# Optimization experiments

Measured on AMD Instinct MI355X. Metric: run time of the kernel, lower is better.

## Reference

```python
import jax, jax.numpy as jnp
import numpy as np

MODES = 32
WIDTH = 64


def crelu(z):
    # split-complex ReLU (torch.relu is undefined on complex; this is the standard fix)
    return jax.nn.relu(z.real) + 1j * jax.nn.relu(z.imag)


def _linear_params(key, fan_in, fan_out):
    k1, k2 = jax.random.split(key)
    s = 1.0 / np.sqrt(fan_in)
    W = jax.random.uniform(k1, (fan_out, fan_in), minval=-s, maxval=s, dtype=jnp.float32)
    b = jax.random.uniform(k2, (fan_out,), minval=-s, maxval=s, dtype=jnp.float32)
    return W, b


def setup_inputs() -> dict:
    key = jax.random.key(0)
    ks = jax.random.split(key, 8)
    B, G = 32768, 512
    H0, H1, H2 = 1024, 512, 64  # hidden_layers; H2 == WIDTH
    FD = 128                    # field_dim
    geometry_input = jax.random.normal(ks[0], (B, G), dtype=jnp.float32)
    W_in, b_in = _linear_params(ks[1], G, H0)
    W_h1, b_h1 = _linear_params(ks[2], H0, H1)
    W_h2, b_h2 = _linear_params(ks[3], H1, H2)
    w0 = jax.random.normal(ks[4], (MODES, WIDTH), dtype=jnp.float32)
    w1 = jax.random.normal(ks[5], (MODES, WIDTH), dtype=jnp.float32)
    lin1_W, lin1_b = _linear_params(ks[6], WIDTH, WIDTH)
    k7a, k7b = jax.random.split(ks[7])
    lin2_W, lin2_b = _linear_params(k7a, WIDTH, WIDTH)
    W_out, b_out = _linear_params(k7b, H2, FD)
    return dict(geometry_input=geometry_input, W_in=W_in, b_in=b_in,
                W_h1=W_h1, b_h1=b_h1, W_h2=W_h2, b_h2=b_h2,
                w0=w0, w1=w1, lin1_W=lin1_W, lin1_b=lin1_b,
                lin2_W=lin2_W, lin2_b=lin2_b, W_out=W_out, b_out=b_out)


def reference(geometry_input, W_in, b_in, W_h1, b_h1, W_h2, b_h2,
              w0, w1, lin1_W, lin1_b, lin2_W, lin2_b, W_out, b_out):
    # MLP encoder: [B, G] -> [B, 64]
    x = jax.nn.relu(geometry_input @ W_in.T + b_in)
    x = jax.nn.relu(x @ W_h1.T + b_h1)
    x = jax.nn.relu(x @ W_h2.T + b_h2)
    # FNO block
    xh = jnp.fft.fftn(x)  # fftn over ALL axes, as in torch code -> complex64 [B, 64]
    phase = jnp.exp(1j * 2.0 * jnp.pi * jnp.arange(MODES) / MODES).astype(jnp.complex64)
    y = xh[:, None, :] * w0  # per-mode lift: [B, MODES, WIDTH]
    y = crelu(y)
    y = y * phase[None, :, None]  # diagonal L mode-multiply
    y = jnp.einsum('bmw,mw->bw', y, w1.astype(y.dtype))  # collapse modes -> [B, WIDTH]
    y = crelu(y @ lin1_W.T + lin1_b)  # real weights on complex acts
    y = y @ lin2_W.T + lin2_b
    y = jnp.fft.ifftn(y)  # [B, 64] complex
    out = y @ W_out.T + b_out  # [B, field_dim] complex
    return out
```

## Files before the change

kernel.cpp:

```cpp
#include <hip/hip_runtime.h>
#include <hip/hip_bf16.h>


#define PI2F 6.28318530717958647692f

typedef __attribute__((ext_vector_type(8))) short short8;
typedef __attribute__((ext_vector_type(4))) float f32x4;

__device__ __forceinline__ unsigned short f2bf(float f) {
  unsigned int u = __float_as_uint(f);
  u += 0x7fff + ((u >> 16) & 1);
  return (unsigned short)(u >> 16);
}
__device__ __forceinline__ unsigned int pack_bf16x2(float a, float b) {
  return (unsigned int)f2bf(a) | ((unsigned int)f2bf(b) << 16);
}

__device__ __forceinline__ void gl2lds16(const void* gptr, const void* lptr) {
  __builtin_amdgcn_global_load_lds(
      (const __attribute__((address_space(1))) unsigned int*)(unsigned long long)gptr,
      (__attribute__((address_space(3))) unsigned int*)(unsigned int)(unsigned long long)lptr,
      16, 0, 0);
}

__global__ __launch_bounds__(256) void f32_to_bf16_k(
    const float* __restrict__ src, unsigned short* __restrict__ dst, int n4)
{
  int i = blockIdx.x * 256 + threadIdx.x;
  if (i < n4) {
    float4 v = ((const float4*)src)[i];
    uint2 p;
    p.x = pack_bf16x2(v.x, v.y);
    p.y = pack_bf16x2(v.z, v.w);
    ((uint2*)dst)[i] = p;
  }
}

template<int BM, int BN, int WM, int WN, typename OUT>
__global__ __launch_bounds__(256) void gemm_async(
    const unsigned short* __restrict__ A, const unsigned short* __restrict__ Bw,
    const float* __restrict__ bias, OUT* __restrict__ C,
    int M, int N, int K)
{
  constexpr int BK = 64;
  __shared__ __align__(16) unsigned short lA[BM * BK];
  __shared__ __align__(16) unsigned short lB[BN * BK];
  const int tid = threadIdx.x;
  const int lane = tid & 63;
  const int wv = tid >> 6;
  const int q = lane >> 4, lr = lane & 15;
  const int x7 = lr & 7;
  constexpr int WN_CNT = BN / WN;
  const int wm = (wv / WN_CNT) * WM;
  const int wn = (wv % WN_CNT) * WN;
  const size_t m0 = (size_t)blockIdx.x * BM;
  const size_t n0 = (size_t)blockIdx.y * BN;
  constexpr int MI = WM / 16, NI = WN / 16;
  f32x4 acc[MI][NI] = {};
  constexpr int A_INSTR = BM * BK / 512;
  constexpr int B_INSTR = BN * BK / 512;
  constexpr int A_PW = A_INSTR / 4, B_PW = B_INSTR / 4;
  (void)M;

  for (int k0 = 0; k0 < K; k0 += BK) {
    __syncthreads();
    #pragma unroll
    for (int s = 0; s < A_PW; ++s) {
      int instr = wv * A_PW + s;
      int pc = instr * 64 + lane;
      int row = pc >> 3, col = pc & 7;
      int lc = col ^ (row & 7);
      gl2lds16(A + (m0 + row) * K + k0 + lc * 8, lA + instr * 512);
    }
    #pragma unroll
    for (int s = 0; s < B_PW; ++s) {
      int instr = wv * B_PW + s;
      int pc = instr * 64 + lane;
      int row = pc >> 3, col = pc & 7;
      int lc = col ^ (row & 7);
      gl2lds16(Bw + (n0 + row) * K + k0 + lc * 8, lB + instr * 512);
    }
    __syncthreads();
    #pragma unroll
    for (int t = 0; t < 2; ++t) {
      short8 af[MI], bfr[NI];
      #pragma unroll
      for (int i = 0; i < MI; ++i) {
        int r = wm + i * 16 + lr;
        af[i] = *(const short8*)(lA + r * 64 + (((t << 2) | q) ^ x7) * 8);
      }
      #pragma unroll
      for (int j = 0; j < NI; ++j) {
        int r = wn + j * 16 + lr;
        bfr[j] = *(const short8*)(lB + r * 64 + (((t << 2) | q) ^ x7) * 8);
      }
      #pragma unroll
      for (int i = 0; i < MI; ++i)
        #pragma unroll
        for (int j = 0; j < NI; ++j)
          acc[i][j] = __builtin_amdgcn_mfma_f32_16x16x32_bf16(af[i], bfr[j], acc[i][j], 0, 0, 0);
    }
  }
  #pragma unroll
  for (int i = 0; i < MI; ++i)
    #pragma unroll
    for (int j = 0; j < NI; ++j) {
      size_t col = n0 + wn + j * 16 + lr;
      float bv = bias[col];
      #pragma unroll
      for (int r = 0; r < 4; ++r) {
        size_t row = m0 + wm + i * 16 + q * 4 + r;
        float v = acc[i][j][r] + bv;
        v = v > 0.f ? v : 0.f;
        if (sizeof(OUT) == 2) ((unsigned short*)C)[row * N + col] = f2bf(v);
        else                  ((float*)C)[row * N + col] = v;
      }
    }
}

__global__ __launch_bounds__(256) void precompute(
    const float* __restrict__ w0, const float* __restrict__ w1,
    const float* __restrict__ l2W, const float* __restrict__ l2b,
    float2* __restrict__ Ap, float2* __restrict__ Am,
    float2* __restrict__ Qt, float2* __restrict__ b2c)
{
  const int t = threadIdx.x;
  const int blk = blockIdx.x;
  if (blk == 0) {
    if (t < 64) {
      float apx = 0, apy = 0, amx = 0, amy = 0;
      for (int m = 0; m < 32; ++m) {
        float s0 = w0[m * 64 + t];
        float cf = w1[m * 64 + t] * s0;
        float sn, cs; sincosf(PI2F * (float)m / 32.f, &sn, &cs);
        if (s0 > 0.f)      { apx += cs * cf; apy += sn * cf; }
        else if (s0 < 0.f) { amx += cs * cf; amy += sn * cf; }
      }
      Ap[t] = make_float2(apx, apy);
      Am[t] = make_float2(amx, amy);
      float bx = 0, by = 0;
      for (int k = 0; k < 64; ++k) {
        float sn, cs; sincosf(PI2F * (float)((t * k) & 63) / 64.f, &sn, &cs);
        float lb = l2b[k] * (1.f / 64.f);
        bx += cs * lb; by += sn * lb;
      }
      b2c[t] = make_float2(bx, by);
    }
  } else {
    int e = (blk - 1) * 256 + t;
    int j = e >> 6, w = e & 63;
    float qx = 0, qy = 0;
    for (int k = 0; k < 64; ++k) {
      float sn, cs; sincosf(PI2F * (float)((j * k) & 63) / 64.f, &sn, &cs);
      float lw = l2W[k * 64 + w] * (1.f / 64.f);
      qx += cs * lw; qy += sn * lw;
    }
    Qt[w * 64 + j] = make_float2(qx, qy);
  }
}

__global__ __launch_bounds__(256) void dft64_rows(
    const float* __restrict__ x3, float2* __restrict__ xh1)
{
  __shared__ __align__(16) float xt[32][64];
  __shared__ float2 tw[64];
  const int t = threadIdx.x;
  const size_t b0 = (size_t)blockIdx.x * 32;
  for (int it = 0; it < 8; ++it) {
    int idx = it * 256 + t;
    int r = idx >> 6, w = idx & 63;
    xt[r][w] = x3[(b0 + r) * 64 + w];
  }
  if (t < 64) {
    float sn, cs; sincosf(-PI2F * (float)t / 64.f, &sn, &cs);
    tw[t] = make_float2(cs, sn);
  }
  __syncthreads();
  const int k = t & 63, rg = t >> 6;
  float2 acc[8] = {};
  #pragma unroll 1
  for (int w4 = 0; w4 < 16; ++w4) {
    int w = 4 * w4;
    int kw = k * w;
    float2 t0 = tw[kw & 63];
    float2 t1 = tw[(kw + k) & 63];
    float2 t2 = tw[(kw + 2 * k) & 63];
    float2 t3 = tw[(kw + 3 * k) & 63];
    #pragma unroll
    for (int r = 0; r < 8; ++r) {
      float4 xv = *(const float4*)(&xt[rg * 8 + r][w]);
      acc[r].x += xv.x * t0.x + xv.y * t1.x + xv.z * t2.x + xv.w * t3.x;
      acc[r].y += xv.x * t0.y + xv.y * t1.y + xv.z * t2.y + xv.w * t3.y;
    }
  }
  #pragma unroll
  for (int r = 0; r < 8; ++r)
    xh1[(b0 + rg * 8 + r) * 64 + k] = acc[r];
}

template<int SIGN>
__global__ __launch_bounds__(256) void fft_stage1(
    const float2* __restrict__ Xin, float2* __restrict__ T)
{
  __shared__ float2 tile[128 * 33];
  __shared__ float2 tw16s[16];
  const int blk = blockIdx.x;
  const int b2 = blk >> 1, wh = (blk & 1) * 32;
  const int t = threadIdx.x;
  for (int it = 0; it < 16; ++it) {
    int idx = it * 256 + t;
    int b1 = idx >> 5, wi = idx & 31;
    tile[b1 * 33 + wi] = Xin[((size_t)(b1 * 256 + b2)) * 64 + wh + wi];
  }
  if (t < 16) {
    float sn, cs; sincosf(SIGN * PI2F * (float)t / 16.f, &sn, &cs);
    tw16s[t] = make_float2(cs, sn);
  }
  __syncthreads();
  const int p = t >> 1, n2a = p >> 4, k1pa = p & 15, w0 = (t & 1) * 16;
  float2 ya[16] = {};
  #pragma unroll 1
  for (int n1 = 0; n1 < 16; ++n1) {
    float2 tv = tw16s[(n1 * k1pa) & 15];
    const float2* row = &tile[(8 * n1 + n2a) * 33 + w0];
    #pragma unroll
    for (int w = 0; w < 16; ++w) {
      float2 d = row[w];
      ya[w].x += d.x * tv.x - d.y * tv.y;
      ya[w].y += d.x * tv.y + d.y * tv.x;
    }
  }
  {
    float sn, cs; sincosf(SIGN * PI2F * (float)(n2a * k1pa) / 128.f, &sn, &cs);
    #pragma unroll
    for (int w = 0; w < 16; ++w) {
      float2 a = ya[w];
      ya[w] = make_float2(a.x * cs - a.y * sn, a.x * sn + a.y * cs);
    }
  }
  __syncthreads();
  {
    float2* yrow = &tile[(n2a * 16 + k1pa) * 33 + w0];
    #pragma unroll
    for (int w = 0; w < 16; ++w) yrow[w] = ya[w];
  }
  __syncthreads();
  const int wB = t & 31, qB = t >> 5;
  float sstep, cstep;
  sincosf(SIGN * PI2F * (float)(16 * b2) / 32768.f, &sstep, &cstep);
  #pragma unroll 1
  for (int h = 0; h < 2; ++h) {
    const int k1p = qB + 8 * h;
    float2 acc[8] = {};
    #pragma unroll 1
    for (int n2 = 0; n2 < 8; ++n2) {
      float2 d = tile[(n2 * 16 + k1p) * 33 + wB];
      #pragma unroll
      for (int k2p = 0; k2p < 8; ++k2p) {
        float2 tv = tw16s[(2 * n2 * k2p) & 15];
        acc[k2p].x += d.x * tv.x - d.y * tv.y;
        acc[k2p].y += d.x * tv.y + d.y * tv.x;
      }
    }
    float sb, cb;
    sincosf(SIGN * PI2F * (float)(b2 * k1p) / 32768.f, &sb, &cb);
    float2 rot = make_float2(cb, sb);
    #pragma unroll
    for (int k2p = 0; k2p < 8; ++k2p) {
      int k1 = k1p + 16 * k2p;
      float2 a = acc[k2p];
      float2 o = make_float2(a.x * rot.x - a.y * rot.y,
                             a.x * rot.y + a.y * rot.x);
      T[((size_t)k1 * 256 + b2) * 64 + wh + wB] = o;
      float nrx = rot.x * cstep - rot.y * sstep;
      rot.y = rot.x * sstep + rot.y * cstep;
      rot.x = nrx;
    }
  }
}

template<int SIGN, bool SCALE>
__global__ __launch_bounds__(256) void fft_stage2(
    const float2* __restrict__ T, float2* __restrict__ X)
{
  __shared__ float2 tile[256 * 17];
  __shared__ float2 tw16s[16];
  const int blk = blockIdx.x;
  const int k1 = blk >> 2, wq = (blk & 3) * 16;
  const int t = threadIdx.x;
  for (int it = 0; it < 16; ++it) {
    int idx = it * 256 + t;
    int r2 = idx >> 4, wi = idx & 15;
    tile[r2 * 17 + wi] = T[((size_t)k1 * 256 + r2) * 64 + wq + wi];
  }
  if (t < 16) {
    float sn, cs; sincosf(SIGN * PI2F * (float)t / 16.f, &sn, &cs);
    tw16s[t] = make_float2(cs, sn);
  }
  __syncthreads();
  const int n2a = t >> 4, k1pa = t & 15;
  float2 ya[16] = {};
  #pragma unroll 1
  for (int n1 = 0; n1 < 16; ++n1) {
    float2 tv = tw16s[(n1 * k1pa) & 15];
    const float2* row = &tile[(16 * n1 + n2a) * 17];
    #pragma unroll
    for (int w = 0; w < 16; ++w) {
      float2 d = row[w];
      ya[w].x += d.x * tv.x - d.y * tv.y;
      ya[w].y += d.x * tv.y + d.y * tv.x;
    }
  }
  {
    float sn, cs; sincosf(SIGN * PI2F * (float)(n2a * k1pa) / 256.f, &sn, &cs);
    #pragma unroll
    for (int w = 0; w < 16; ++w) {
      float2 a = ya[w];
      ya[w] = make_float2(a.x * cs - a.y * sn, a.x * sn + a.y * cs);
    }
  }
  __syncthreads();
  {
    float2* yrow = &tile[(n2a * 16 + k1pa) * 17];
    #pragma unroll
    for (int w = 0; w < 16; ++w) yrow[w] = ya[w];
  }
  __syncthreads();
  const int k1pb = t >> 4, wB = t & 15;
  float2 acc[16] = {};
  #pragma unroll 1
  for (int n2 = 0; n2 < 16; ++n2) {
    float2 d = tile[(n2 * 16 + k1pb) * 17 + wB];
    #pragma unroll
    for (int k2p = 0; k2p < 16; ++k2p) {
      float2 tv = tw16s[(n2 * k2p) & 15];
      acc[k2p].x += d.x * tv.x - d.y * tv.y;
      acc[k2p].y += d.x * tv.y + d.y * tv.x;
    }
  }
  const float sc = SCALE ? (1.f / 32768.f) : 1.f;
  #pragma unroll
  for (int k2p = 0; k2p < 16; ++k2p) {
    int k2 = k1pb + 16 * k2p;
    size_t row = (size_t)(k1 + 128 * k2);
    X[row * 64 + wq + wB] = make_float2(acc[k2p].x * sc, acc[k2p].y * sc);
  }
}

__global__ __launch_bounds__(256) void pw_lin(
    const float2* __restrict__ xh,
    const float2* __restrict__ Ap, const float2* __restrict__ Am,
    const float* __restrict__ l1W, const float* __restrict__ l1b,
    const float2* __restrict__ Qt, const float2* __restrict__ b2c,
    float2* __restrict__ u)
{
  __shared__ __align__(16) float2 tile[32][64];
  __shared__ __align__(16) float2 qt[64 * 64];
  const int t = threadIdx.x;
  const int lane = t & 63;
  const int wv = t >> 6;
  const size_t b0 = (size_t)blockIdx.x * 32;

  #pragma unroll
  for (int s = 0; s < 8; ++s) {
    int instr = wv * 8 + s;
    gl2lds16((const char*)Qt + instr * 1024 + lane * 16,
             (const char*)qt + instr * 1024);
  }

  for (int it = 0; it < 8; ++it) {
    int idx = it * 256 + t;
    int r = idx >> 6, w = idx & 63;
    float2 xv = xh[(b0 + r) * 64 + w];
    float2 Aa = (xv.x >= 0.f) ? Ap[w] : Am[w];
    float2 Ab = (xv.y >= 0.f) ? Ap[w] : Am[w];
    tile[r][w] = make_float2(xv.x * Aa.x - xv.y * Ab.y,
                             xv.x * Aa.y + xv.y * Ab.x);
  }
  __syncthreads();

  const int n = lane, rg = wv;

  {
    float2 acc[8] = {};
    const float* wrow = l1W + n * 64;
    float4 lwn = *(const float4*)wrow;
    #pragma unroll 1
    for (int w2 = 0; w2 < 16; ++w2) {
      float4 lw = lwn;
      lwn = *(const float4*)(wrow + 4 * ((w2 + 1) & 15));
      int w = 4 * w2;
      #pragma unroll
      for (int r = 0; r < 8; ++r) {
        const float4* rowp = (const float4*)(&tile[rg * 8 + r][w]);
        float4 y01 = rowp[0];
        float4 y23 = rowp[1];
        acc[r].x += y01.x * lw.x + y01.z * lw.y + y23.x * lw.z + y23.z * lw.w;
        acc[r].y += y01.y * lw.x + y01.w * lw.y + y23.y * lw.z + y23.w * lw.w;
      }
    }
    float bb = l1b[n];
    #pragma unroll
    for (int r = 0; r < 8; ++r) {
      float zr = acc[r].x + bb; zr = zr > 0.f ? zr : 0.f;
      float zi = acc[r].y;      zi = zi > 0.f ? zi : 0.f;
      tile[rg * 8 + r][n] = make_float2(zr, zi);
    }
  }

  {
    const int j = lane;
    float2 acc[8] = {};
    #pragma unroll 1
    for (int w2 = 0; w2 < 16; ++w2) {
      int w = 4 * w2;
      float2 q0 = qt[(w + 0) * 64 + j];
      float2 q1 = qt[(w + 1) * 64 + j];
      float2 q2 = qt[(w + 2) * 64 + j];
      float2 q3 = qt[(w + 3) * 64 + j];
      #pragma unroll
      for (int r = 0; r < 8; ++r) {
        const float4* rowp = (const float4*)(&tile[rg * 8 + r][w]);
        float4 z01 = rowp[0];
        float4 z23 = rowp[1];
        acc[r].x += z01.x * q0.x - z01.y * q0.y
                  + z01.z * q1.x - z01.w * q1.y
                  + z23.x * q2.x - z23.y * q2.y
                  + z23.z * q3.x - z23.w * q3.y;
        acc[r].y += z01.x * q0.y + z01.y * q0.x
                  + z01.z * q1.y + z01.w * q1.x
                  + z23.x * q2.y + z23.y * q2.x
                  + z23.z * q3.y + z23.w * q3.x;
      }
    }
    float2 bc = b2c[j];
    #pragma unroll
    for (int r = 0; r < 8; ++r)
      u[(b0 + rg * 8 + r) * 64 + j] = make_float2(acc[r].x + bc.x, acc[r].y + bc.y);
  }
}

template<int MODE>
__global__ __launch_bounds__(256) void final_out(
    const float2* __restrict__ v, const float* __restrict__ Wout,
    const float* __restrict__ bout, float* __restrict__ out)
{
  __shared__ __align__(16) float2 vt[32][64];
  const int t = threadIdx.x;
  const size_t b0 = (size_t)blockIdx.x * 32;
  for (int it = 0; it < 8; ++it) {
    int idx = it * 256 + t;
    int r = idx >> 6, w = idx & 63;
    vt[r][w] = v[(b0 + r) * 64 + w];
  }
  __syncthreads();
  const int f = t & 127, rg = t >> 7;
  const float* wrow = Wout + f * 64;
  float2 acc[16] = {};
  float2 wvn = *(const float2*)wrow;
  #pragma unroll 1
  for (int j2 = 0; j2 < 32; ++j2) {
    float2 wc = wvn;
    wvn = *(const float2*)(wrow + 2 * ((j2 + 1) & 31));
    #pragma unroll
    for (int r = 0; r < 16; ++r) {
      float4 vv = *(const float4*)(&vt[rg * 16 + r][2 * j2]);
      acc[r].x += vv.x * wc.x + vv.z * wc.y;
      acc[r].y += vv.y * wc.x + vv.w * wc.y;
    }
  }
  float bb = bout[f];
  #pragma unroll
  for (int r = 0; r < 16; ++r) {
    size_t idx = (b0 + rg * 16 + r) * 128 + f;
    if (MODE == 0) out[idx] = acc[r].x + bb;
    else ((float2*)out)[idx] = make_float2(acc[r].x + bb, acc[r].y);
  }
}

extern "C" void kernel_launch(void* const* d_in, const int* in_sizes, int n_in,
                              void* d_out, int out_size, void* d_ws, size_t ws_size,
                              hipStream_t stream)
{
  (void)in_sizes; (void)n_in; (void)ws_size;
  const float* geom = (const float*)d_in[0];
  const float* Win  = (const float*)d_in[1];
  const float* bin  = (const float*)d_in[2];
  const float* Wh1  = (const float*)d_in[3];
  const float* bh1  = (const float*)d_in[4];
  const float* Wh2  = (const float*)d_in[5];
  const float* bh2  = (const float*)d_in[6];
  const float* w0   = (const float*)d_in[7];
  const float* w1   = (const float*)d_in[8];
  const float* l1W  = (const float*)d_in[9];
  const float* l1b  = (const float*)d_in[10];
  const float* l2W  = (const float*)d_in[11];
  const float* l2b  = (const float*)d_in[12];
  const float* Wout = (const float*)d_in[13];
  const float* bout = (const float*)d_in[14];

  char* ws = (char*)d_ws;
  const size_t MB = 1048576ull;
  unsigned short* geomb = (unsigned short*)(ws);
  unsigned short* x2b   = (unsigned short*)(ws);
  unsigned short* x1b   = (unsigned short*)(ws + 32 * MB);
  float*  x3  = (float*)(ws + 32 * MB);
  float2* S0  = (float2*)(ws + 40 * MB);
  float2* S1  = (float2*)(ws + 56 * MB);
  float2* Ap  = (float2*)(ws + 72 * MB);
  float2* Am  = (float2*)(ws + 72 * MB + 512);
  float2* b2c = (float2*)(ws + 72 * MB + 1024);
  float2* Qt  = (float2*)(ws + 72 * MB + 1536);
  unsigned short* Winb = (unsigned short*)(ws + 96 * MB);
  unsigned short* Wh1b = (unsigned short*)(ws + 97 * MB);
  unsigned short* Wh2b = (unsigned short*)(ws + 98 * MB);

  f32_to_bf16_k<<<16384, 256, 0, stream>>>(geom, geomb, 4194304);
  f32_to_bf16_k<<<512, 256, 0, stream>>>(Win, Winb, 131072);
  f32_to_bf16_k<<<512, 256, 0, stream>>>(Wh1, Wh1b, 131072);
  f32_to_bf16_k<<<32, 256, 0, stream>>>(Wh2, Wh2b, 8192);

  gemm_async<128,128,64,64,unsigned short><<<dim3(256, 8), 256, 0, stream>>>(
      geomb, Winb, bin, x1b, 32768, 1024, 512);
  gemm_async<128,128,64,64,unsigned short><<<dim3(256, 4), 256, 0, stream>>>(
      x1b, Wh1b, bh1, x2b, 32768, 512, 1024);
  gemm_async<128, 64,64,32,float><<<dim3(256, 1), 256, 0, stream>>>(
      x2b, Wh2b, bh2, x3, 32768, 64, 512);

  precompute<<<17, 256, 0, stream>>>(w0, w1, l2W, l2b, Ap, Am, Qt, b2c);
  dft64_rows<<<1024, 256, 0, stream>>>(x3, S0);
  fft_stage1<-1><<<512, 256, 0, stream>>>(S0, S1);
  fft_stage2<-1, false><<<512, 256, 0, stream>>>(S1, S0);
  pw_lin<<<1024, 256, 0, stream>>>(S0, Ap, Am, l1W, l1b, Qt, b2c, S1);
  fft_stage1<1><<<512, 256, 0, stream>>>(S1, S0);
  fft_stage2<1, true><<<512, 256, 0, stream>>>(S0, S1);
  if (out_size >= 8388608) {
    final_out<1><<<1024, 256, 0, stream>>>(S1, Wout, bout, (float*)d_out);
  } else {
    final_out<0><<<1024, 256, 0, stream>>>(S1, Wout, bout, (float*)d_out);
  }
}
```

Before: 450.2 us.

## Add 256x256 double-buffered bf16 MFMA GEMM for the two large encoder layers

Introduces a new GEMM kernel with 256x256 output tiles, 512 threads (8 waves, each owning a 128x64 sub-tile) and double-buffered LDS staged through global_load_lds with an XOR swizzle. MFMA bursts are wrapped in s_setprio. It replaces the 128x128 kernel for the first two MLP layers. The goal is more operand reuse per LDS byte and overlap of the next tile's loads with current compute. The cost is 128 KB of LDS per block, so each CU likely runs only one block, and fewer blocks are launched, which can leave CUs partly idle in the last wave.

```diff
diff --git a/kernel.cpp b/kernel.cpp
--- a/kernel.cpp
+++ b/kernel.cpp
@@ -34,6 +34,100 @@
     p.y = pack_bf16x2(v.z, v.w);
     ((uint2*)dst)[i] = p;
   }
+}
+
+template<typename OUT>
+__global__ __launch_bounds__(512, 2) void gemm256_db(
+    const unsigned short* __restrict__ A, const unsigned short* __restrict__ Bw,
+    const float* __restrict__ bias, OUT* __restrict__ C,
+    int N, int K)
+{
+  constexpr int BM = 256, BN = 256, BK = 64;
+  __shared__ __align__(16) unsigned short lds[2 * (BM + BN) * BK];
+  const int tid = threadIdx.x;
+  const int lane = tid & 63;
+  const int wv = tid >> 6;
+  const int q = lane >> 4, lr = lane & 15;
+  const int x7 = lr & 7;
+  const int wm = (wv >> 2) * 128;
+  const int wn = (wv & 3) * 64;
+  const size_t m0 = (size_t)blockIdx.x * BM;
+  const size_t n0 = (size_t)blockIdx.y * BN;
+  constexpr int MI = 8, NI = 4;
+  f32x4 acc[MI][NI] = {};
+
+  auto STAGE = [&](int c, int kk) {
+    unsigned short* dA = lds + c * (BM + BN) * BK;
+    unsigned short* dB = dA + BM * BK;
+    #pragma unroll
+    for (int s = 0; s < 4; ++s) {
+      int instr = wv * 4 + s;
+      int pc = instr * 64 + lane;
+      int row = pc >> 3, col = pc & 7;
+      int lc = col ^ (row & 7);
+      gl2lds16(A + (m0 + row) * (size_t)K + kk + lc * 8, dA + instr * 512);
+    }
+    #pragma unroll
+    for (int s = 0; s < 4; ++s) {
+      int instr = wv * 4 + s;
+      int pc = instr * 64 + lane;
+      int row = pc >> 3, col = pc & 7;
+      int lc = col ^ (row & 7);
+      gl2lds16(Bw + (n0 + row) * (size_t)K + kk + lc * 8, dB + instr * 512);
+    }
+  };
+
+  auto COMPUTE = [&](int c) {
+    const unsigned short* sA = lds + c * (BM + BN) * BK;
+    const unsigned short* sB = sA + BM * BK;
+    #pragma unroll
+    for (int t2 = 0; t2 < 2; ++t2) {
+      short8 af[MI], bfr[NI];
+      #pragma unroll
+      for (int i = 0; i < MI; ++i) {
+        int r = wm + i * 16 + lr;
+        af[i] = *(const short8*)(sA + r * 64 + (((t2 << 2) | q) ^ x7) * 8);
+      }
+      #pragma unroll
+      for (int j = 0; j < NI; ++j) {
+        int r = wn + j * 16 + lr;
+        bfr[j] = *(const short8*)(sB + r * 64 + (((t2 << 2) | q) ^ x7) * 8);
+      }
+      __builtin_amdgcn_s_setprio(1);
+      #pragma unroll
+      for (int i = 0; i < MI; ++i)
+        #pragma unroll
+        for (int j = 0; j < NI; ++j)
+          acc[i][j] = __builtin_amdgcn_mfma_f32_16x16x32_bf16(af[i], bfr[j], acc[i][j], 0, 0, 0);
+      __builtin_amdgcn_s_setprio(0);
+    }
+  };
+
+  const int nt = K / BK;
+  STAGE(0, 0);
+  __syncthreads();
+  for (int t = 0; t < nt; ++t) {
+    int cur = t & 1;
+    if (t + 1 < nt) STAGE(cur ^ 1, (t + 1) * BK);
+    COMPUTE(cur);
+    __syncthreads();
+  }
+
+  #pragma unroll
+  for (int i = 0; i < MI; ++i)
+    #pragma unroll
+    for (int j = 0; j < NI; ++j) {
+      size_t col = n0 + wn + j * 16 + lr;
+      float bv = bias[col];
+      #pragma unroll
+      for (int r = 0; r < 4; ++r) {
+        size_t row = m0 + wm + i * 16 + q * 4 + r;
+        float v = acc[i][j][r] + bv;
+        v = v > 0.f ? v : 0.f;
+        if (sizeof(OUT) == 2) ((unsigned short*)C)[row * N + col] = f2bf(v);
+        else                  ((float*)C)[row * N + col] = v;
+      }
+    }
 }
 
 template<int BM, int BN, int WM, int WN, typename OUT>
@@ -520,10 +614,10 @@
   f32_to_bf16_k<<<512, 256, 0, stream>>>(Wh1, Wh1b, 131072);
   f32_to_bf16_k<<<32, 256, 0, stream>>>(Wh2, Wh2b, 8192);
 
-  gemm_async<128,128,64,64,unsigned short><<<dim3(256, 8), 256, 0, stream>>>(
-      geomb, Winb, bin, x1b, 32768, 1024, 512);
-  gemm_async<128,128,64,64,unsigned short><<<dim3(256, 4), 256, 0, stream>>>(
-      x1b, Wh1b, bh1, x2b, 32768, 512, 1024);
+  gemm256_db<unsigned short><<<dim3(128, 4), 512, 0, stream>>>(
+      geomb, Winb, bin, x1b, 1024, 512);
+  gemm256_db<unsigned short><<<dim3(128, 2), 512, 0, stream>>>(
+      x1b, Wh1b, bh1, x2b, 512, 1024);
   gemm_async<128, 64,64,32,float><<<dim3(256, 1), 256, 0, stream>>>(
       x2b, Wh2b, bh2, x3, 32768, 64, 512);
 
```

Result: faster. 436.6 us (-3.0%).

## Add triple-buffered 128x256 GEMM kernel for first two MLP layers

Applied to the files above, without the earlier changes.

Introduces gemm_pipe, a 512-thread, 128x256-tile bf16 MFMA GEMM with a three-stage LDS ring fed by async global-to-LDS loads. Loads for the tile two steps ahead are issued in halves between the MFMA phases, and MFMA phases run at raised wave priority. Workgroup indices are remapped with an XCD-aware swizzle. It replaces gemm_async for the two large encoder layers, aiming to hide memory latency and improve operand reuse, at the cost of more LDS per block and one block per CU.

```diff
diff --git a/kernel.cpp b/kernel.cpp
--- a/kernel.cpp
+++ b/kernel.cpp
@@ -34,6 +34,130 @@
     p.y = pack_bf16x2(v.z, v.w);
     ((uint2*)dst)[i] = p;
   }
+}
+
+template<int NBLOG, typename OUT>
+__global__ __launch_bounds__(512, 1) void gemm_pipe(
+    const unsigned short* __restrict__ A, const unsigned short* __restrict__ Bw,
+    const float* __restrict__ bias, OUT* __restrict__ C, int N, int K)
+{
+  constexpr int BM = 128, BN = 256, BK = 64;
+  constexpr int ASZ = BM * BK;
+  constexpr int BSZ = BN * BK;
+  constexpr int BUF = ASZ + BSZ;
+  __shared__ __align__(16) unsigned short lds[3 * BUF];
+
+  const int nwg = gridDim.x;
+  const int cpx = nwg >> 3;
+  const int orig = blockIdx.x;
+  const int wg = (orig & 7) * cpx + (orig >> 3);
+  const int mb = wg >> NBLOG;
+  const int nb = wg & ((1 << NBLOG) - 1);
+  const size_t m0 = (size_t)mb * BM;
+  const size_t n0 = (size_t)nb * BN;
+
+  const int tid = threadIdx.x;
+  const int lane = tid & 63;
+  const int wv = tid >> 6;
+  const int q = lane >> 4, lr = lane & 15;
+  const int x7 = lr & 7;
+  const int wm = (wv >> 2) * 64;
+  const int wn = (wv & 3) * 64;
+  f32x4 acc[4][4] = {};
+
+  auto STAGE_HALF = [&](int r, int kk, int s0) {
+    unsigned short* dA = lds + r * BUF;
+    #pragma unroll
+    for (int u = 0; u < 3; ++u) {
+      int e = wv * 6 + s0 + u;
+      int isA = (e < 16) ? 1 : 0;
+      int e2 = isA ? e : e - 16;
+      int pc = e2 * 64 + lane;
+      int row = pc >> 3, col = pc & 7;
+      int lc = col ^ (row & 7);
+      const unsigned short* src = isA ? A : Bw;
+      size_t rb = isA ? m0 : n0;
+      unsigned short* dst = dA + (isA ? 0 : ASZ) + e2 * 512;
+      gl2lds16(src + (rb + row) * (size_t)K + kk + lc * 8, dst);
+    }
+  };
+
+  const int nt = K / BK;
+  STAGE_HALF(0, 0, 0); STAGE_HALF(0, 0, 3);
+  STAGE_HALF(1, BK, 0); STAGE_HALF(1, BK, 3);
+  asm volatile("s_waitcnt vmcnt(6)" ::: "memory");
+  __builtin_amdgcn_s_barrier();
+
+  int r0 = 0;
+  for (int t = 0; t < nt; ++t) {
+    const unsigned short* sA = lds + r0 * BUF;
+    const unsigned short* sB = sA + ASZ;
+    const bool st = (t + 2) < nt;
+    const int r2 = (r0 >= 1) ? (r0 - 1) : 2;
+    const int kk2 = (t + 2) * BK;
+
+    short8 af[4][2], bf0[2][2];
+    #pragma unroll
+    for (int i = 0; i < 4; ++i)
+      #pragma unroll
+      for (int t2 = 0; t2 < 2; ++t2)
+        af[i][t2] = *(const short8*)(sA + (wm + i * 16 + lr) * 64 + (((t2 << 2) | q) ^ x7) * 8);
+    #pragma unroll
+    for (int j = 0; j < 2; ++j)
+      #pragma unroll
+      for (int t2 = 0; t2 < 2; ++t2)
+        bf0[j][t2] = *(const short8*)(sB + (wn + j * 16 + lr) * 64 + (((t2 << 2) | q) ^ x7) * 8);
+    if (st) STAGE_HALF(r2, kk2, 0);
+    __builtin_amdgcn_s_setprio(1);
+    #pragma unroll
+    for (int i = 0; i < 4; ++i)
+      #pragma unroll
+      for (int j = 0; j < 2; ++j)
+        #pragma unroll
+        for (int t2 = 0; t2 < 2; ++t2)
+          acc[i][j] = __builtin_amdgcn_mfma_f32_16x16x32_bf16(af[i][t2], bf0[j][t2], acc[i][j], 0, 0, 0);
+    __builtin_amdgcn_s_setprio(0);
+    __builtin_amdgcn_s_barrier();
+
+    short8 bf1[2][2];
+    #pragma unroll
+    for (int j = 0; j < 2; ++j)
+      #pragma unroll
+      for (int t2 = 0; t2 < 2; ++t2)
+        bf1[j][t2] = *(const short8*)(sB + (wn + (j + 2) * 16 + lr) * 64 + (((t2 << 2) | q) ^ x7) * 8);
+    if (st) STAGE_HALF(r2, kk2, 3);
+    __builtin_amdgcn_s_setprio(1);
+    #pragma unroll
+    for (int i = 0; i < 4; ++i)
+      #pragma unroll
+      for (int j = 0; j < 2; ++j)
+        #pragma unroll
+        for (int t2 = 0; t2 < 2; ++t2)
+          acc[i][j + 2] = __builtin_amdgcn_mfma_f32_16x16x32_bf16(af[i][t2], bf1[j][t2], acc[i][j + 2], 0, 0, 0);
+    __builtin_amdgcn_s_setprio(0);
+
+    asm volatile("s_waitcnt lgkmcnt(0)" ::: "memory");
+    if (st) { asm volatile("s_waitcnt vmcnt(6)" ::: "memory"); }
+    else    { asm volatile("s_waitcnt vmcnt(0)" ::: "memory"); }
+    __builtin_amdgcn_s_barrier();
+    r0 = (r0 + 1 >= 3) ? 0 : r0 + 1;
+  }
+
+  #pragma unroll
+  for (int i = 0; i < 4; ++i)
+    #pragma unroll
+    for (int j = 0; j < 4; ++j) {
+      size_t col = n0 + wn + j * 16 + lr;
+      float bv = bias[col];
+      #pragma unroll
+      for (int r = 0; r < 4; ++r) {
+        size_t row = m0 + wm + i * 16 + q * 4 + r;
+        float v = acc[i][j][r] + bv;
+        v = v > 0.f ? v : 0.f;
+        if (sizeof(OUT) == 2) ((unsigned short*)C)[row * N + col] = f2bf(v);
+        else                  ((float*)C)[row * N + col] = v;
+      }
+    }
 }
 
 template<int BM, int BN, int WM, int WN, typename OUT>
@@ -520,10 +644,10 @@
   f32_to_bf16_k<<<512, 256, 0, stream>>>(Wh1, Wh1b, 131072);
   f32_to_bf16_k<<<32, 256, 0, stream>>>(Wh2, Wh2b, 8192);
 
-  gemm_async<128,128,64,64,unsigned short><<<dim3(256, 8), 256, 0, stream>>>(
-      geomb, Winb, bin, x1b, 32768, 1024, 512);
-  gemm_async<128,128,64,64,unsigned short><<<dim3(256, 4), 256, 0, stream>>>(
-      x1b, Wh1b, bh1, x2b, 32768, 512, 1024);
+  gemm_pipe<2, unsigned short><<<1024, 512, 0, stream>>>(
+      geomb, Winb, bin, x1b, 1024, 512);
+  gemm_pipe<1, unsigned short><<<512, 512, 0, stream>>>(
+      x1b, Wh1b, bh1, x2b, 512, 1024);
   gemm_async<128, 64,64,32,float><<<dim3(256, 1), 256, 0, stream>>>(
       x2b, Wh2b, bh2, x3, 32768, 64, 512);
 
```

Result: no change. 443.5 us (-1.5%).
